# Kernel tuning notes

Hardware: AMD Instinct MI355X
Metric: run time of the kernel (lower is better)

Reference implementation:

```python
import jax, jax.numpy as jnp
import numpy as np

C = 256          # channels
NH = 8           # heads
DH = 64          # dim_head
NMEM = 4         # num_mem_kv
HIDDEN = NH * DH # 512
SCALE = DH ** (-0.5)


def _rmsnorm(x, gain):
    # F.normalize(x, dim=1) * gain * sqrt(C)  (scale-only RMS norm over channel dim)
    n = jnp.sqrt(jnp.sum(x * x, axis=1, keepdims=True))
    return x / jnp.maximum(n, 1e-12) * gain * (x.shape[1] ** 0.5)


def setup_inputs() -> dict:
    key = jax.random.key(0)
    ks = jax.random.split(key, 6)
    B, Hh, Ww = 16, 64, 64
    return {
        "x": jax.random.normal(ks[0], (B, C, Hh, Ww), jnp.float32),
        "gain1": jnp.ones((1, C, 1, 1), jnp.float32),
        "w_qkv": jax.random.normal(ks[1], (3 * HIDDEN, C), jnp.float32) * 0.02,
        "mem_kv": jax.random.normal(ks[2], (2, NH, DH, NMEM), jnp.float32),
        "w_out": jax.random.normal(ks[3], (C, HIDDEN), jnp.float32) * 0.02,
        "b_out": jnp.zeros((C,), jnp.float32),
        "gain2": jnp.ones((1, C, 1, 1), jnp.float32),
    }


def reference(x, gain1, w_qkv, mem_kv, w_out, b_out, gain2):
    B, _, Hh, Ww = x.shape
    N = Hh * Ww
    # pre-norm
    xn = _rmsnorm(x, gain1)
    # 1x1 conv QKV projection (no bias) == channel GEMM
    qkv = jnp.einsum('oc,bchw->bohw', w_qkv, xn)          # [B, 3*hidden, H, W]
    qkv = qkv.reshape(B, 3, NH, DH, N)                    # chunk + 'b (h c) x y -> b h c (x y)'
    q, k, v = qkv[:, 0], qkv[:, 1], qkv[:, 2]             # [B, h, d, N]
    # learned global memory kv, broadcast over batch
    mem_k = jnp.broadcast_to(mem_kv[0], (B, NH, DH, NMEM))
    mem_v = jnp.broadcast_to(mem_kv[1], (B, NH, DH, NMEM))
    k = jnp.concatenate([mem_k, k], axis=-1)              # [B, h, d, NMEM+N]
    v = jnp.concatenate([mem_v, v], axis=-1)
    # dual softmax: q over feature dim d, k over token dim n
    q = jax.nn.softmax(q, axis=-2) * SCALE
    k = jax.nn.softmax(k, axis=-1)
    # linear attention: O(N) context
    context = jnp.einsum('bhdn,bhen->bhde', k, v)         # [B, h, d, e]
    out = jnp.einsum('bhde,bhdn->bhen', context, q)       # [B, h, e, N]
    out = out.reshape(B, HIDDEN, Hh, Ww)
    # 1x1 conv out projection (with bias) + post RMSNorm
    out = jnp.einsum('oc,bchw->bohw', w_out, out) + b_out[None, :, None, None]
    return _rmsnorm(out, gain2)
```

## Files before the change

### kernel.cpp

```cpp
#include <hip/hip_runtime.h>

typedef __attribute__((ext_vector_type(8))) short bf16x8;
typedef __attribute__((ext_vector_type(4))) short bf16x4;
typedef __attribute__((ext_vector_type(4))) float f32x4;
typedef unsigned short u16;

constexpr int B_   = 16;
constexpr int C_   = 256;
constexpr int NH   = 8;
constexpr int DH   = 64;
constexpr int NMEM = 4;
constexpr int HID  = 512;
constexpr int QKVC = 1536;
constexpr int N_   = 4096;
constexpr int CTXS = 4224;

__device__ __forceinline__ u16 f2b(float f) {
  union { float f; unsigned u; } v{f};
  unsigned r = v.u + 0x7fff + ((v.u >> 16) & 1);
  return (u16)(r >> 16);
}
__device__ __forceinline__ float b2f(u16 h) {
  union { unsigned u; float f; } v; v.u = ((unsigned)h) << 16; return v.f;
}

__device__ __forceinline__ void gld_lds16(const u16* g, u16* l) {
  __builtin_amdgcn_global_load_lds(
      (const __attribute__((address_space(1))) unsigned*)g,
      (__attribute__((address_space(3))) unsigned*)l, 16, 0, 0);
}

__global__ void k_cvtw(const float* __restrict__ wq, const float* __restrict__ wo,
                       u16* __restrict__ wqb, u16* __restrict__ wob) {
  int i = blockIdx.x * 256 + threadIdx.x;
  for (int idx = i; idx < QKVC * C_; idx += gridDim.x * 256) wqb[idx] = f2b(wq[idx]);
  for (int idx = i; idx < C_ * HID; idx += gridDim.x * 256) wob[idx] = f2b(wo[idx]);
}

__global__ __launch_bounds__(256) void k_rms1(const float* __restrict__ x,
                                              const float* __restrict__ g1,
                                              u16* __restrict__ xbT) {
  int g = blockIdx.y;
  int n = blockIdx.x * 64 + (threadIdx.x & 63);
  int ch = threadIdx.x >> 6;
  __shared__ float ssp[4][64];
  __shared__ float invs[64];
  const float* xp = x + (size_t)g * C_ * N_ + n;
  float ss = 0.f;
  #pragma unroll 16
  for (int c = ch * 64; c < ch * 64 + 64; ++c) {
    float v = xp[(size_t)c * N_];
    ss += v * v;
  }
  ssp[ch][n & 63] = ss;
  __syncthreads();
  if (threadIdx.x < 64) {
    float tot = (ssp[0][threadIdx.x] + ssp[1][threadIdx.x]) +
                (ssp[2][threadIdx.x] + ssp[3][threadIdx.x]);
    invs[threadIdx.x] = 16.0f / fmaxf(sqrtf(tot), 1e-12f);
  }
  __syncthreads();
  float inv = invs[n & 63];
  u16* op = xbT + ((size_t)g * N_ + n) * C_;
  #pragma unroll 2
  for (int c0 = ch * 64; c0 < ch * 64 + 64; c0 += 8) {
    union { bf16x8 v; u16 u[8]; } pk;
    #pragma unroll
    for (int j = 0; j < 8; ++j) pk.u[j] = f2b(xp[(size_t)(c0 + j) * N_] * inv * g1[c0 + j]);
    *(bf16x8*)(op + c0) = pk.v;
  }
}

__global__ __launch_bounds__(256) void k_kvctx(const u16* __restrict__ Wb,
                                               const u16* __restrict__ XT,
                                               float* __restrict__ ctxp) {
  __shared__ __align__(16) u16 smem[16384];
  u16* Ws = smem;
  u16* Xs = smem + 8192;
  u16* Pl = smem;
  u16* Vl = smem + 8192;

  int cpx = gridDim.x >> 3;
  int bid = blockIdx.x;
  int L = (bid & 7) * cpx + (bid >> 3);
  int h = L & 7, nc = (L >> 3) & 7, g = L >> 6;
  int t = threadIdx.x, wave = t >> 6, lane = t & 63;
  int wm = wave >> 1, wn = wave & 1;
  int kg = lane >> 4, lr = lane & 15;

  const u16* WK = Wb + (size_t)(HID + h * DH) * C_;
  const u16* WV = Wb + (size_t)(2 * HID + h * DH) * C_;
  const u16* Xg = XT + ((size_t)g * N_ + nc * 512) * C_;

  int rl8 = lane >> 3;
  int cs8 = (lane & 7) ^ rl8;
  const u16* Wsrc = (wave < 2) ? WK : WV;

  f32x4 acc2[4];
  #pragma unroll
  for (int nf = 0; nf < 4; ++nf) acc2[nf] = (f32x4)0.f;
  float rs[4] = {0.f, 0.f, 0.f, 0.f};

  for (int it = 0; it < 4; ++it) {
    f32x4 acc[4][4];
    #pragma unroll
    for (int i = 0; i < 4; ++i)
      #pragma unroll
      for (int j = 0; j < 4; ++j) acc[i][j] = (f32x4)0.f;

    for (int k0 = 0; k0 < C_; k0 += 64) {
      #pragma unroll
      for (int q = 0; q < 4; ++q) {
        int rb = wave * 32 + q * 8;
        int rw = (rb & 63) + rl8;
        int rx = it * 128 + rb + rl8;
        gld_lds16(Wsrc + (size_t)rw * C_ + k0 + cs8 * 8, Ws + rb * 64);
        gld_lds16(Xg + (size_t)rx * C_ + k0 + cs8 * 8, Xs + rb * 64);
      }
      __syncthreads();
      #pragma unroll
      for (int ks = 0; ks < 2; ++ks) {
        int ch = ks * 4 + kg;
        bf16x8 a[4], bv[4];
        #pragma unroll
        for (int mf = 0; mf < 4; ++mf) {
          int r = wm * 64 + mf * 16 + lr;
          a[mf] = *(const bf16x8*)(Xs + r * 64 + ((ch ^ (r & 7)) * 8));
        }
        #pragma unroll
        for (int nf = 0; nf < 4; ++nf) {
          int r = wn * 64 + nf * 16 + lr;
          bv[nf] = *(const bf16x8*)(Ws + r * 64 + ((ch ^ (r & 7)) * 8));
        }
        #pragma unroll
        for (int mf = 0; mf < 4; ++mf)
          #pragma unroll
          for (int nf = 0; nf < 4; ++nf)
            acc[mf][nf] = __builtin_amdgcn_mfma_f32_16x16x32_bf16(a[mf], bv[nf], acc[mf][nf], 0, 0, 0);
      }
      __syncthreads();
    }

    if (wn == 0) {
      #pragma unroll
      for (int mf = 0; mf < 4; ++mf) {
        int nb = wm * 64 + mf * 16 + kg * 4;
        int cc = nb >> 3, off = nb & 7;
        #pragma unroll
        for (int nf = 0; nf < 4; ++nf) {
          int d = nf * 16 + lr;
          float e0 = __expf(acc[mf][nf][0]);
          float e1 = __expf(acc[mf][nf][1]);
          float e2 = __expf(acc[mf][nf][2]);
          float e3 = __expf(acc[mf][nf][3]);
          rs[nf] += (e0 + e1) + (e2 + e3);
          union { bf16x4 v; u16 u[4]; } pk;
          pk.u[0] = f2b(e0); pk.u[1] = f2b(e1); pk.u[2] = f2b(e2); pk.u[3] = f2b(e3);
          *(bf16x4*)(Pl + d * 128 + ((cc ^ (d & 15)) * 8) + off) = pk.v;
        }
      }
    } else {
      #pragma unroll
      for (int mf = 0; mf < 4; ++mf) {
        int nb = wm * 64 + mf * 16 + kg * 4;
        int cc = nb >> 3, off = nb & 7;
        #pragma unroll
        for (int nf = 0; nf < 4; ++nf) {
          int e = nf * 16 + lr;
          union { bf16x4 v; u16 u[4]; } pk;
          pk.u[0] = f2b(acc[mf][nf][0]); pk.u[1] = f2b(acc[mf][nf][1]);
          pk.u[2] = f2b(acc[mf][nf][2]); pk.u[3] = f2b(acc[mf][nf][3]);
          *(bf16x4*)(Vl + e * 128 + ((cc ^ (e & 15)) * 8) + off) = pk.v;
        }
      }
    }
    __syncthreads();

    #pragma unroll
    for (int k = 0; k < 4; ++k) {
      int c = k * 4 + kg;
      bf16x8 af = *(const bf16x8*)(Pl + (wave * 16 + lr) * 128 + ((c ^ lr) * 8));
      #pragma unroll
      for (int nf = 0; nf < 4; ++nf) {
        bf16x8 bfv = *(const bf16x8*)(Vl + (nf * 16 + lr) * 128 + ((c ^ lr) * 8));
        acc2[nf] = __builtin_amdgcn_mfma_f32_16x16x32_bf16(af, bfv, acc2[nf], 0, 0, 0);
      }
    }
    __syncthreads();
  }

  float* cgp = ctxp + ((size_t)(g * NH + h) * 8 + nc) * CTXS;
  #pragma unroll
  for (int nf = 0; nf < 4; ++nf)
    #pragma unroll
    for (int j = 0; j < 4; ++j) {
      int d = wave * 16 + kg * 4 + j;
      int e = nf * 16 + lr;
      cgp[d * 64 + e] = acc2[nf][j];
    }
  if (wn == 0) {
    #pragma unroll
    for (int nf = 0; nf < 4; ++nf) {
      rs[nf] += __shfl_xor(rs[nf], 16);
      rs[nf] += __shfl_xor(rs[nf], 32);
    }
    if (lane < 16) {
      #pragma unroll
      for (int nf = 0; nf < 4; ++nf)
        cgp[4096 + wm * 64 + nf * 16 + lane] = rs[nf];
    }
  }
}

__global__ __launch_bounds__(256) void k_cwo(const float* __restrict__ ctxp,
                                             const float* __restrict__ memkv,
                                             const u16* __restrict__ Wo,
                                             u16* __restrict__ wo2) {
  int g = blockIdx.y, h = blockIdx.x;
  int t = threadIdx.x, wave = t >> 6, lane = t & 63;
  int kg = lane >> 4, lr = lane & 15;
  int rl8 = lane >> 3, cs8 = (lane & 7) ^ rl8;
  __shared__ float emk[DH * NMEM];
  __shared__ float sd[DH];
  __shared__ __align__(16) u16 Cl[64 * 64];
  __shared__ __align__(16) u16 As2[256 * 64];

  const float* mk = memkv + (size_t)h * DH * NMEM;
  const float* mv = memkv + (size_t)(NH + h) * DH * NMEM;
  const float* cp = ctxp + (size_t)(g * NH + h) * 8 * CTXS;
  emk[t] = __expf(mk[t]);
  __syncthreads();
  if (t < DH) {
    float s = 0.f;
    #pragma unroll
    for (int p = 0; p < 8; ++p)
      s += cp[p * CTXS + 4096 + t] + cp[p * CTXS + 4160 + t];
    #pragma unroll
    for (int j = 0; j < NMEM; ++j) s += emk[t * 4 + j];
    sd[t] = s;
  }
  #pragma unroll
  for (int q = 0; q < 8; ++q) {
    int rb = wave * 64 + q * 8;
    gld_lds16(Wo + (size_t)(rb + rl8) * HID + h * DH + cs8 * 8, As2 + rb * 64);
  }
  __syncthreads();
  #pragma unroll
  for (int i = 0; i < 16; ++i) {
    int idx = t + 256 * i;
    int d = idx >> 6, e = idx & 63;
    float v = 0.f;
    #pragma unroll
    for (int p = 0; p < 8; ++p) v += cp[p * CTXS + idx];
    #pragma unroll
    for (int j = 0; j < NMEM; ++j) v += emk[d * 4 + j] * mv[e * 4 + j];
    Cl[d * 64 + (((e >> 3) ^ (d & 7)) * 8) + (e & 7)] = f2b(v / sd[d]);
  }
  __syncthreads();
  f32x4 acc[4][4];
  #pragma unroll
  for (int i = 0; i < 4; ++i)
    #pragma unroll
    for (int j = 0; j < 4; ++j) acc[i][j] = (f32x4)0.f;
  #pragma unroll
  for (int ks = 0; ks < 2; ++ks) {
    int ch = ks * 4 + kg;
    bf16x8 a[4], b[4];
    #pragma unroll
    for (int mf = 0; mf < 4; ++mf) {
      int r = wave * 64 + mf * 16 + lr;
      a[mf] = *(const bf16x8*)(As2 + r * 64 + ((ch ^ (r & 7)) * 8));
    }
    #pragma unroll
    for (int nf = 0; nf < 4; ++nf) {
      int rd = nf * 16 + lr;
      b[nf] = *(const bf16x8*)(Cl + rd * 64 + ((ch ^ (rd & 7)) * 8));
    }
    #pragma unroll
    for (int mf = 0; mf < 4; ++mf)
      #pragma unroll
      for (int nf = 0; nf < 4; ++nf)
        acc[mf][nf] = __builtin_amdgcn_mfma_f32_16x16x32_bf16(a[mf], b[nf], acc[mf][nf], 0, 0, 0);
  }
  u16* og = wo2 + (size_t)g * 256 * 512;
  #pragma unroll
  for (int mf = 0; mf < 4; ++mf)
    #pragma unroll
    for (int nf = 0; nf < 4; ++nf)
      #pragma unroll
      for (int j = 0; j < 4; ++j) {
        int c = wave * 64 + mf * 16 + kg * 4 + j;
        int dd = nf * 16 + lr;
        og[(size_t)c * 512 + h * DH + dd] = f2b(acc[mf][nf][j]);
      }
}

__global__ __launch_bounds__(512) void k_qout(const u16* __restrict__ Wq,
                                              const u16* __restrict__ XT,
                                              const u16* __restrict__ Wo2,
                                              const float* __restrict__ bias,
                                              const float* __restrict__ g2,
                                              float* __restrict__ out) {
  __shared__ __align__(16) u16 smem[32768];
  u16* R0 = smem;
  u16* R1 = smem + 16384;

  int cpx = gridDim.x >> 3;
  int bid = blockIdx.x;
  int L = (bid & 7) * cpx + (bid >> 3);
  int nc = L & 63, g = L >> 6;
  int t = threadIdx.x, wave = t >> 6, lane = t & 63;
  int kg = lane >> 4, lr = lane & 15;
  int rl4 = lane >> 2, cs4 = (lane & 3) ^ (rl4 & 3);
  int rl8 = lane >> 3, cs8 = (lane & 7) ^ rl8;

  const u16* Xg = XT + ((size_t)g * N_ + nc * 64) * C_;
  const u16* W2g = Wo2 + (size_t)g * 256 * 512;

  {
    int xrow_off = lane >> 5;
    int c32 = lane & 31;
    #pragma unroll
    for (int q = 0; q < 4; ++q) {
      int base = wave * 8 + q * 2;
      int row = base + xrow_off;
      int sw = (c32 & 24) | ((c32 & 7) ^ (row & 7));
      gld_lds16(Xg + (size_t)row * C_ + sw * 8, R1 + base * 256);
    }
  }

  f32x4 acc[4][4];
  #pragma unroll
  for (int i = 0; i < 4; ++i)
    #pragma unroll
    for (int j = 0; j < 4; ++j) acc[i][j] = (f32x4)0.f;

  for (int k0i = 0; k0i < 8; ++k0i) {
    int k0 = k0i * 32;
    #pragma unroll
    for (int q = 0; q < 4; ++q) {
      int rb = ((wave * 4 + q) & 31) * 16;
      gld_lds16(Wq + (size_t)(rb + rl4) * C_ + k0 + cs4 * 8, R0 + rb * 32);
    }
    __syncthreads();
    bf16x8 a[4], bv[4];
    #pragma unroll
    for (int mf = 0; mf < 4; ++mf) {
      int r = wave * 64 + mf * 16 + lr;
      a[mf] = *(const bf16x8*)(R0 + r * 32 + ((kg ^ (r & 3)) * 8));
    }
    #pragma unroll
    for (int nf = 0; nf < 4; ++nf) {
      int bn = nf * 16 + lr;
      int c32 = k0i * 4 + kg;
      int sw = (c32 & 24) | ((c32 & 7) ^ (bn & 7));
      bv[nf] = *(const bf16x8*)(R1 + bn * 256 + sw * 8);
    }
    #pragma unroll
    for (int mf = 0; mf < 4; ++mf)
      #pragma unroll
      for (int nf = 0; nf < 4; ++nf)
        acc[mf][nf] = __builtin_amdgcn_mfma_f32_16x16x32_bf16(a[mf], bv[nf], acc[mf][nf], 0, 0, 0);
    __syncthreads();
  }

  float colsum[4];
  #pragma unroll
  for (int nf = 0; nf < 4; ++nf) {
    float s = 0.f;
    #pragma unroll
    for (int mf = 0; mf < 4; ++mf)
      #pragma unroll
      for (int j = 0; j < 4; ++j) {
        float e = __expf(acc[mf][nf][j]);
        acc[mf][nf][j] = e;
        s += e;
      }
    colsum[nf] = s;
  }
  #pragma unroll
  for (int nf = 0; nf < 4; ++nf) {
    colsum[nf] += __shfl_xor(colsum[nf], 16);
    colsum[nf] += __shfl_xor(colsum[nf], 32);
    colsum[nf] = 0.125f / colsum[nf];
  }

  f32x4 acc2[2][4];
  #pragma unroll
  for (int i = 0; i < 2; ++i)
    #pragma unroll
    for (int j = 0; j < 4; ++j) acc2[i][j] = (f32x4)0.f;

  #pragma unroll
  for (int half = 0; half < 2; ++half) {
    if ((wave >> 2) == half) {
      #pragma unroll
      for (int nf = 0; nf < 4; ++nf) {
        int n = nf * 16 + lr;
        float invs = colsum[nf];
        #pragma unroll
        for (int mf = 0; mf < 4; ++mf)
          #pragma unroll
          for (int jp = 0; jp < 2; ++jp) {
            int oc = (wave & 3) * 64 + mf * 16 + kg * 4 + jp * 2;
            u16 lo = f2b(acc[mf][nf][jp * 2] * invs);
            u16 hi = f2b(acc[mf][nf][jp * 2 + 1] * invs);
            unsigned pk = (unsigned)lo | ((unsigned)hi << 16);
            int c8 = oc >> 3;
            int sw = (c8 & 24) | ((c8 & 7) ^ (n & 7));
            *(unsigned*)(R1 + n * 256 + sw * 8 + (oc & 7)) = pk;
          }
      }
    }
    __syncthreads();
    for (int k0l = 0; k0l < 4; ++k0l) {
      int cb = half * 256 + k0l * 64;
      #pragma unroll
      for (int q = 0; q < 4; ++q) {
        int rb = ((wave * 4 + q) & 31) * 8;
        gld_lds16(W2g + (size_t)(rb + rl8) * 512 + cb + cs8 * 8, R0 + rb * 64);
      }
      __syncthreads();
      #pragma unroll
      for (int ks = 0; ks < 2; ++ks) {
        int ch = ks * 4 + kg;
        bf16x8 a2[2], b2[4];
        #pragma unroll
        for (int mf = 0; mf < 2; ++mf) {
          int r = wave * 32 + mf * 16 + lr;
          a2[mf] = *(const bf16x8*)(R0 + r * 64 + ((ch ^ (r & 7)) * 8));
        }
        #pragma unroll
        for (int nf = 0; nf < 4; ++nf) {
          int bn = nf * 16 + lr;
          int c8 = k0l * 8 + ks * 4 + kg;
          int sw = (c8 & 24) | ((c8 & 7) ^ (bn & 7));
          b2[nf] = *(const bf16x8*)(R1 + bn * 256 + sw * 8);
        }
        #pragma unroll
        for (int mf = 0; mf < 2; ++mf)
          #pragma unroll
          for (int nf = 0; nf < 4; ++nf)
            acc2[mf][nf] = __builtin_amdgcn_mfma_f32_16x16x32_bf16(a2[mf], b2[nf], acc2[mf][nf], 0, 0, 0);
      }
      __syncthreads();
    }
  }

  float colsq[4] = {0.f, 0.f, 0.f, 0.f};
  #pragma unroll
  for (int mf = 0; mf < 2; ++mf)
    #pragma unroll
    for (int j = 0; j < 4; ++j) {
      int c = wave * 32 + mf * 16 + kg * 4 + j;
      float bs = bias[c];
      #pragma unroll
      for (int nf = 0; nf < 4; ++nf) {
        float v = acc2[mf][nf][j] + bs;
        acc2[mf][nf][j] = v;
        colsq[nf] += v * v;
      }
    }
  #pragma unroll
  for (int nf = 0; nf < 4; ++nf) {
    colsq[nf] += __shfl_xor(colsq[nf], 16);
    colsq[nf] += __shfl_xor(colsq[nf], 32);
  }
  float* part = (float*)R0;
  if (kg == 0) {
    #pragma unroll
    for (int nf = 0; nf < 4; ++nf) part[wave * 64 + nf * 16 + lr] = colsq[nf];
  }
  __syncthreads();
  float* og = out + (size_t)g * C_ * N_ + nc * 64;
  #pragma unroll
  for (int nf = 0; nf < 4; ++nf) {
    int col = nf * 16 + lr;
    float tot = 0.f;
    #pragma unroll
    for (int w = 0; w < 8; ++w) tot += part[w * 64 + col];
    float invn = 16.0f / fmaxf(sqrtf(tot), 1e-12f);
    #pragma unroll
    for (int mf = 0; mf < 2; ++mf)
      #pragma unroll
      for (int j = 0; j < 4; ++j) {
        int c = wave * 32 + mf * 16 + kg * 4 + j;
        og[(size_t)c * N_ + col] = acc2[mf][nf][j] * invn * g2[c];
      }
  }
}

extern "C" void kernel_launch(void* const* d_in, const int* in_sizes, int n_in,
                              void* d_out, int out_size, void* d_ws, size_t ws_size,
                              hipStream_t stream) {
  (void)in_sizes; (void)n_in; (void)out_size;
  const float* x      = (const float*)d_in[0];
  const float* gain1  = (const float*)d_in[1];
  const float* w_qkv  = (const float*)d_in[2];
  const float* mem_kv = (const float*)d_in[3];
  const float* w_out  = (const float*)d_in[4];
  const float* b_out  = (const float*)d_in[5];
  const float* gain2  = (const float*)d_in[6];
  float* out = (float*)d_out;

  char* ws = (char*)d_ws;
  u16* wqkvb = (u16*)ws;
  u16* woutb = (u16*)(ws + 786432);
  size_t shared_b = 1048576;

  const size_t xbT_b  = (size_t)N_ * C_ * 2;
  const size_t ctxp_b = (size_t)NH * 8 * CTXS * 4;
  const size_t wo2_b  = (size_t)256 * 512 * 2;
  const size_t per_b  = xbT_b + ctxp_b + wo2_b;

  int G = 16;
  while (G > 1 && shared_b + (size_t)G * per_b > ws_size) G >>= 1;

  char* base = ws + shared_b;
  u16*   xbT  = (u16*)base;
  float* ctxp = (float*)(base + (size_t)G * xbT_b);
  u16*   wo2  = (u16*)(base + (size_t)G * (xbT_b + ctxp_b));

  k_cvtw<<<256, 256, 0, stream>>>(w_qkv, w_out, wqkvb, woutb);

  for (int b0 = 0; b0 < B_; b0 += G) {
    const float* xc = x + (size_t)b0 * C_ * N_;
    float*       oc = out + (size_t)b0 * C_ * N_;
    k_rms1  <<<dim3(N_ / 64, G),   256, 0, stream>>>(xc, gain1, xbT);
    k_kvctx <<<dim3(64 * G),       256, 0, stream>>>(wqkvb, xbT, ctxp);
    k_cwo   <<<dim3(NH, G),        256, 0, stream>>>(ctxp, mem_kv, woutb, wo2);
    k_qout  <<<dim3(64 * G),       512, 0, stream>>>(wqkvb, xbT, wo2, b_out, gain2, oc);
  }
}
```

Baseline: 172.1 us.

## Widen k_qout token tile to 128 with 16 waves sharing weight tiles

The fused Q-softmax and output-projection kernel now processes 128 tokens per block instead of 64. It uses 1024 threads, so 16 waves split into two token halves that share the same Wq and Wo2 tiles staged in LDS. This halves the weight global-to-LDS traffic per token and halves the grid size. The bf16 packing of the normalized q is hoisted into registers before the store loop. The cost is more LDS per block (96KB) and tighter register limits from the 1024-thread launch bound, which may cut occupancy or cause spills.

```diff
diff --git a/kernel.cpp b/kernel.cpp
--- a/kernel.cpp
+++ b/kernel.cpp
@@ -295,26 +295,27 @@
       }
 }
 
-__global__ __launch_bounds__(512) void k_qout(const u16* __restrict__ Wq,
-                                              const u16* __restrict__ XT,
-                                              const u16* __restrict__ Wo2,
-                                              const float* __restrict__ bias,
-                                              const float* __restrict__ g2,
-                                              float* __restrict__ out) {
-  __shared__ __align__(16) u16 smem[32768];
+__global__ __launch_bounds__(1024) void k_qout(const u16* __restrict__ Wq,
+                                               const u16* __restrict__ XT,
+                                               const u16* __restrict__ Wo2,
+                                               const float* __restrict__ bias,
+                                               const float* __restrict__ g2,
+                                               float* __restrict__ out) {
+  __shared__ __align__(16) u16 smem[49152];
   u16* R0 = smem;
   u16* R1 = smem + 16384;
 
   int cpx = gridDim.x >> 3;
   int bid = blockIdx.x;
   int L = (bid & 7) * cpx + (bid >> 3);
-  int nc = L & 63, g = L >> 6;
+  int nc = L & 31, g = L >> 5;
   int t = threadIdx.x, wave = t >> 6, lane = t & 63;
   int kg = lane >> 4, lr = lane & 15;
   int rl4 = lane >> 2, cs4 = (lane & 3) ^ (rl4 & 3);
   int rl8 = lane >> 3, cs8 = (lane & 7) ^ rl8;
-
-  const u16* Xg = XT + ((size_t)g * N_ + nc * 64) * C_;
+  int hq = wave & 7, nh2 = wave >> 3;
+
+  const u16* Xg = XT + ((size_t)g * N_ + nc * 128) * C_;
   const u16* W2g = Wo2 + (size_t)g * 256 * 512;
 
   {
@@ -338,20 +339,20 @@
   for (int k0i = 0; k0i < 8; ++k0i) {
     int k0 = k0i * 32;
     #pragma unroll
-    for (int q = 0; q < 4; ++q) {
-      int rb = ((wave * 4 + q) & 31) * 16;
+    for (int q = 0; q < 2; ++q) {
+      int rb = ((wave * 2 + q) & 31) * 16;
       gld_lds16(Wq + (size_t)(rb + rl4) * C_ + k0 + cs4 * 8, R0 + rb * 32);
     }
     __syncthreads();
     bf16x8 a[4], bv[4];
     #pragma unroll
     for (int mf = 0; mf < 4; ++mf) {
-      int r = wave * 64 + mf * 16 + lr;
+      int r = hq * 64 + mf * 16 + lr;
       a[mf] = *(const bf16x8*)(R0 + r * 32 + ((kg ^ (r & 3)) * 8));
     }
     #pragma unroll
     for (int nf = 0; nf < 4; ++nf) {
-      int bn = nf * 16 + lr;
+      int bn = nh2 * 64 + nf * 16 + lr;
       int c32 = k0i * 4 + kg;
       int sw = (c32 & 24) | ((c32 & 7) ^ (bn & 7));
       bv[nf] = *(const bf16x8*)(R1 + bn * 256 + sw * 8);
@@ -384,7 +385,21 @@
     colsum[nf] += __shfl_xor(colsum[nf], 32);
     colsum[nf] = 0.125f / colsum[nf];
   }
-
+  unsigned pq[4][4][2];
+  #pragma unroll
+  for (int nf = 0; nf < 4; ++nf) {
+    float invs = colsum[nf];
+    #pragma unroll
+    for (int mf = 0; mf < 4; ++mf)
+      #pragma unroll
+      for (int jp = 0; jp < 2; ++jp) {
+        u16 lo = f2b(acc[mf][nf][jp * 2] * invs);
+        u16 hi = f2b(acc[mf][nf][jp * 2 + 1] * invs);
+        pq[mf][nf][jp] = (unsigned)lo | ((unsigned)hi << 16);
+      }
+  }
+
+  int wc = wave & 7;
   f32x4 acc2[2][4];
   #pragma unroll
   for (int i = 0; i < 2; ++i)
@@ -393,22 +408,18 @@
 
   #pragma unroll
   for (int half = 0; half < 2; ++half) {
-    if ((wave >> 2) == half) {
+    if ((hq >> 2) == half) {
       #pragma unroll
       for (int nf = 0; nf < 4; ++nf) {
-        int n = nf * 16 + lr;
-        float invs = colsum[nf];
+        int n = nh2 * 64 + nf * 16 + lr;
         #pragma unroll
         for (int mf = 0; mf < 4; ++mf)
           #pragma unroll
           for (int jp = 0; jp < 2; ++jp) {
-            int oc = (wave & 3) * 64 + mf * 16 + kg * 4 + jp * 2;
-            u16 lo = f2b(acc[mf][nf][jp * 2] * invs);
-            u16 hi = f2b(acc[mf][nf][jp * 2 + 1] * invs);
-            unsigned pk = (unsigned)lo | ((unsigned)hi << 16);
+            int oc = (hq & 3) * 64 + mf * 16 + kg * 4 + jp * 2;
             int c8 = oc >> 3;
             int sw = (c8 & 24) | ((c8 & 7) ^ (n & 7));
-            *(unsigned*)(R1 + n * 256 + sw * 8 + (oc & 7)) = pk;
+            *(unsigned*)(R1 + n * 256 + sw * 8 + (oc & 7)) = pq[mf][nf][jp];
           }
       }
     }
@@ -416,8 +427,8 @@
     for (int k0l = 0; k0l < 4; ++k0l) {
       int cb = half * 256 + k0l * 64;
       #pragma unroll
-      for (int q = 0; q < 4; ++q) {
-        int rb = ((wave * 4 + q) & 31) * 8;
+      for (int q = 0; q < 2; ++q) {
+        int rb = ((wave * 2 + q) & 31) * 8;
         gld_lds16(W2g + (size_t)(rb + rl8) * 512 + cb + cs8 * 8, R0 + rb * 64);
       }
       __syncthreads();
@@ -427,12 +438,12 @@
         bf16x8 a2[2], b2[4];
         #pragma unroll
         for (int mf = 0; mf < 2; ++mf) {
-          int r = wave * 32 + mf * 16 + lr;
+          int r = wc * 32 + mf * 16 + lr;
           a2[mf] = *(const bf16x8*)(R0 + r * 64 + ((ch ^ (r & 7)) * 8));
         }
         #pragma unroll
         for (int nf = 0; nf < 4; ++nf) {
-          int bn = nf * 16 + lr;
+          int bn = nh2 * 64 + nf * 16 + lr;
           int c8 = k0l * 8 + ks * 4 + kg;
           int sw = (c8 & 24) | ((c8 & 7) ^ (bn & 7));
           b2[nf] = *(const bf16x8*)(R1 + bn * 256 + sw * 8);
@@ -452,7 +463,7 @@
   for (int mf = 0; mf < 2; ++mf)
     #pragma unroll
     for (int j = 0; j < 4; ++j) {
-      int c = wave * 32 + mf * 16 + kg * 4 + j;
+      int c = wc * 32 + mf * 16 + kg * 4 + j;
       float bs = bias[c];
       #pragma unroll
       for (int nf = 0; nf < 4; ++nf) {
@@ -472,19 +483,20 @@
     for (int nf = 0; nf < 4; ++nf) part[wave * 64 + nf * 16 + lr] = colsq[nf];
   }
   __syncthreads();
-  float* og = out + (size_t)g * C_ * N_ + nc * 64;
+  float* og = out + (size_t)g * C_ * N_ + nc * 128;
   #pragma unroll
   for (int nf = 0; nf < 4; ++nf) {
-    int col = nf * 16 + lr;
+    int cl_ = nf * 16 + lr;
     float tot = 0.f;
     #pragma unroll
-    for (int w = 0; w < 8; ++w) tot += part[w * 64 + col];
+    for (int w = 0; w < 8; ++w) tot += part[(nh2 * 8 + w) * 64 + cl_];
     float invn = 16.0f / fmaxf(sqrtf(tot), 1e-12f);
+    int col = nh2 * 64 + cl_;
     #pragma unroll
     for (int mf = 0; mf < 2; ++mf)
       #pragma unroll
       for (int j = 0; j < 4; ++j) {
-        int c = wave * 32 + mf * 16 + kg * 4 + j;
+        int c = wc * 32 + mf * 16 + kg * 4 + j;
         og[(size_t)c * N_ + col] = acc2[mf][nf][j] * invn * g2[c];
       }
   }
@@ -529,6 +541,6 @@
     k_rms1  <<<dim3(N_ / 64, G),   256, 0, stream>>>(xc, gain1, xbT);
     k_kvctx <<<dim3(64 * G),       256, 0, stream>>>(wqkvb, xbT, ctxp);
     k_cwo   <<<dim3(NH, G),        256, 0, stream>>>(ctxp, mem_kv, woutb, wo2);
-    k_qout  <<<dim3(64 * G),       512, 0, stream>>>(wqkvb, xbT, wo2, b_out, gain2, oc);
-  }
-}
+    k_qout  <<<dim3(32 * G),       1024, 0, stream>>>(wqkvb, xbT, wo2, b_out, gain2, oc);
+  }
+}
```

After: 161.9 us (median of 2 runs). 5.9% less time.
